# Kernel tuning notes

Hardware: AMD Instinct MI355X
Metric: run time of the kernel (lower is better)

The kernel has to match this reference:

```python
import jax, jax.numpy as jnp
import numpy as np

N = 50000
E = 800000
EMB = 128
HID = 128
HALF = HID // 2

def setup_inputs() -> dict:
    key = jax.random.key(0)
    ks = jax.random.split(key, 16)
    inp = {
        "x": jax.random.normal(ks[0], (N, EMB), dtype=jnp.float32),
        "edge_row": jax.random.randint(ks[1], (E,), 0, N, dtype=jnp.int32),
        "edge_col": jax.random.randint(ks[2], (E,), 0, N, dtype=jnp.int32),
        "edge_vals": jax.random.uniform(ks[3], (E,), dtype=jnp.float32),
        "W_gc0": jax.random.normal(ks[4], (EMB, HID), dtype=jnp.float32) * 0.05,
        "b_gc0": jax.random.normal(ks[5], (HID,), dtype=jnp.float32) * 0.05,
        "W_gc1": jax.random.normal(ks[6], (HID, HID), dtype=jnp.float32) * 0.05,
        "b_gc1": jax.random.normal(ks[7], (HID,), dtype=jnp.float32) * 0.05,
        "Wm1": jax.random.normal(ks[8], (HID, HALF), dtype=jnp.float32) * 0.05,
        "bm1": jax.random.normal(ks[9], (HALF,), dtype=jnp.float32) * 0.05,
        "Wm2": jax.random.normal(ks[10], (HALF, HALF), dtype=jnp.float32) * 0.05,
        "bm2": jax.random.normal(ks[11], (HALF,), dtype=jnp.float32) * 0.05,
        "Wv1": jax.random.normal(ks[12], (HID, HALF), dtype=jnp.float32) * 0.05,
        "bv1": jax.random.normal(ks[13], (HALF,), dtype=jnp.float32) * 0.05,
        "Wv2": jax.random.normal(ks[14], (HALF, HALF), dtype=jnp.float32) * 0.05,
        "bv2": jax.random.normal(ks[15], (HALF,), dtype=jnp.float32) * 0.05,
    }
    return inp

def reference(x, edge_row, edge_col, edge_vals,
              W_gc0, b_gc0, W_gc1, b_gc1,
              Wm1, bm1, Wm2, bm2, Wv1, bv1, Wv2, bv2):
    n = x.shape[0]

    def gcn_layer(h, W, b):
        # support = h @ W  (dense GEMM), then spmm: out[r] += adj[r,c] * support[c]
        support = h @ W                                   # [N, out]
        msgs = edge_vals[:, None] * support[edge_col]      # [E, out]
        agg = jax.ops.segment_sum(msgs, edge_row, num_segments=n)
        return agg + b

    h = jax.nn.relu(gcn_layer(x, W_gc0, b_gc0))
    h = jax.nn.relu(gcn_layer(h, W_gc1, b_gc1))

    mean = jax.nn.relu(h @ Wm1 + bm1) @ Wm2 + bm2
    logvar = jax.nn.relu(h @ Wv1 + bv1) @ Wv2 + bv2
    return mean, logvar
```

## Files before the change

### kernel.cpp

```cpp
#include <hip/hip_runtime.h>
#include <type_traits>


typedef _Float16 half8 __attribute__((ext_vector_type(8)));
typedef float floatx4 __attribute__((ext_vector_type(4)));

#define BCAP 2560
#define CHUNK 2048
#define RB 128

__device__ void gemm_l1(int bid, const float* __restrict__ A,
                        const _Float16* __restrict__ Wswz,
                        _Float16* __restrict__ C0, int n) {
  const int t = threadIdx.x;
  const int lane = t & 63, wave = t >> 6;
  const int quad = lane >> 4, l16 = lane & 15;
  const int r_base = bid * 128 + wave * 32;

  int arow0 = r_base + l16;
  int arow1 = r_base + 16 + l16;
  if (arow0 >= n) arow0 = n - 1;
  if (arow1 >= n) arow1 = n - 1;
  const float* Ap0 = A + (size_t)arow0 * 128 + quad * 8;
  const float* Ap1 = A + (size_t)arow1 * 128 + quad * 8;

  floatx4 acc[2][8] = {};

#pragma unroll
  for (int ks = 0; ks < 4; ++ks) {
    float4 u = *(const float4*)(Ap0 + ks * 32);
    float4 w = *(const float4*)(Ap0 + ks * 32 + 4);
    half8 a0 = half8{(_Float16)u.x, (_Float16)u.y, (_Float16)u.z, (_Float16)u.w,
                     (_Float16)w.x, (_Float16)w.y, (_Float16)w.z, (_Float16)w.w};
    float4 u1 = *(const float4*)(Ap1 + ks * 32);
    float4 w1 = *(const float4*)(Ap1 + ks * 32 + 4);
    half8 a1 = half8{(_Float16)u1.x, (_Float16)u1.y, (_Float16)u1.z, (_Float16)u1.w,
                     (_Float16)w1.x, (_Float16)w1.y, (_Float16)w1.z, (_Float16)w1.w};
#pragma unroll
    for (int nt = 0; nt < 8; ++nt) {
      half8 b = *(const half8*)(Wswz + ((size_t)(ks * 8 + nt) * 64 + lane) * 8);
      acc[0][nt] = __builtin_amdgcn_mfma_f32_16x16x32_f16(a0, b, acc[0][nt], 0, 0, 0);
      acc[1][nt] = __builtin_amdgcn_mfma_f32_16x16x32_f16(a1, b, acc[1][nt], 0, 0, 0);
    }
  }

#pragma unroll
  for (int h = 0; h < 2; ++h) {
#pragma unroll
    for (int nt = 0; nt < 8; ++nt) {
      const int col = nt * 16 + l16;
#pragma unroll
      for (int r = 0; r < 4; ++r) {
        int row = r_base + h * 16 + quad * 4 + r;
        if (row < n) C0[(size_t)row * 128 + col] = (_Float16)acc[h][nt][r];
      }
    }
  }
}

__global__ __launch_bounds__(256)
void buildA_kernel(const int* __restrict__ rows, const int* __restrict__ cols,
                   const float* __restrict__ vals,
                   int* __restrict__ bcur, uint2* __restrict__ bbuf, int e,
                   int binBlocks,
                   const float* __restrict__ w0, const float* __restrict__ w1,
                   const float* __restrict__ wm1, const float* __restrict__ wv1,
                   const float* __restrict__ wm2, const float* __restrict__ wv2,
                   _Float16* __restrict__ d0, _Float16* __restrict__ d1,
                   _Float16* __restrict__ dh1, _Float16* __restrict__ dh2) {
  __shared__ int cnt[392];
  __shared__ int cur[392];
  const int t = threadIdx.x;

  if (blockIdx.x >= binBlocks) {
    int i = (blockIdx.x - binBlocks) * 256 + t;
    if (i >= 65536) return;
    int seg = i >> 14, li = i & 16383;
    int j = li & 7, lane = (li >> 3) & 63, tt = li >> 9;
    int nt = tt & 7, ks = tt >> 3;
    int k = ks * 32 + (lane >> 4) * 8 + j;
    int nn = nt * 16 + (lane & 15);
    float v;
    if (seg == 0)      v = w0[k * 128 + nn];
    else if (seg == 1) v = w1[k * 128 + nn];
    else if (seg == 2) v = (nn < 64) ? wm1[k * 64 + nn] : wv1[k * 64 + (nn - 64)];
    else v = (k < 64 && nn < 64) ? wm2[k * 64 + nn]
           : (k >= 64 && nn >= 64) ? wv2[(k - 64) * 64 + (nn - 64)] : 0.f;
    _Float16* dst = (seg == 0) ? d0 : (seg == 1) ? d1 : (seg == 2) ? dh1 : dh2;
    dst[li] = (_Float16)v;
    return;
  }

  const int lo = blockIdx.x * CHUNK, hi = min(lo + CHUNK, e);
  int myr[8], myc[8];
  float myv[8];
  int nk = 0;
  for (int i = lo + t; i < hi; i += 256, ++nk) {
    myr[nk] = rows[i];
    myc[nk] = cols[i];
    myv[nk] = vals[i];
  }
  for (int j = t; j < 392; j += 256) cnt[j] = 0;
  __syncthreads();
  for (int k = 0; k < nk; ++k)
    atomicAdd(&cnt[myr[k] >> 7], 1);
  __syncthreads();
  for (int j = t; j < 392; j += 256)
    if (cnt[j] > 0) cur[j] = atomicAdd(&bcur[j * 16], cnt[j]);
  __syncthreads();
  for (int k = 0; k < nk; ++k) {
    int r = myr[k];
    int b = r >> 7;
    int p = atomicAdd(&cur[b], 1);
    if (p < BCAP)
      bbuf[(size_t)b * BCAP + p] =
          make_uint2(((unsigned)(r & (RB - 1)) << 16) | (unsigned)myc[k],
                     __float_as_uint(myv[k]));
  }
}

__global__ __launch_bounds__(256)
void buildB_kernel(const uint2* __restrict__ bbuf, const int* __restrict__ bcur,
                   int* __restrict__ row_ptr, int2* __restrict__ s_pack,
                   int nbk, int n, int e_total,
                   const float* __restrict__ x, const _Float16* __restrict__ W0s,
                   _Float16* __restrict__ sup) {
  __shared__ int cnt[RB];
  __shared__ int scn[RB];
  __shared__ int red[256];
  __shared__ int2 stage[BCAP];

  if (blockIdx.x >= nbk) {
    gemm_l1(blockIdx.x - nbk, x, W0s, sup, n);
    return;
  }

  const int b = blockIdx.x, t = threadIdx.x;

  int partial = 0;
  for (int j = t; j < b; j += 256) partial += bcur[j * 16];
  red[t] = partial;
  __syncthreads();
#pragma unroll
  for (int off = 128; off > 0; off >>= 1) {
    if (t < off) red[t] += red[t + off];
    __syncthreads();
  }
  const int base = red[0];

  const int e = min(bcur[b * 16], BCAP);
  const uint2* src = bbuf + (size_t)b * BCAP;

  if (t < RB) cnt[t] = 0;
  __syncthreads();
  for (int i = t; i < e; i += 256)
    atomicAdd(&cnt[(src[i].x >> 16) & (RB - 1)], 1);
  __syncthreads();
  int c = (t < RB) ? cnt[t] : 0;
  if (t < RB) scn[t] = c;
  __syncthreads();
#pragma unroll
  for (int off = 1; off < RB; off <<= 1) {
    int a = (t >= off && t < RB) ? scn[t - off] : 0;
    __syncthreads();
    if (t < RB) scn[t] += a;
    __syncthreads();
  }
  if (t < RB) {
    int excl = scn[t] - c;
    int grow = b * RB + t;
    if (grow < n) row_ptr[grow] = base + excl;
    cnt[t] = excl;
  }
  if (b == 0 && t == 0) row_ptr[n] = e_total;
  __syncthreads();
  for (int i = t; i < e; i += 256) {
    uint2 u = src[i];
    int pos = atomicAdd(&cnt[(u.x >> 16) & (RB - 1)], 1);
    stage[pos] = make_int2((int)(u.x & 0xFFFFu), (int)u.y);
  }
  __syncthreads();
  for (int i = t; i < e; i += 256)
    s_pack[base + i] = stage[i];
}

template<bool HEADS>
__global__ __launch_bounds__(256)
void spmm_fused(const half8* __restrict__ sup, const int* __restrict__ row_ptr,
                const int2* __restrict__ s_pack, const float* __restrict__ gbias,
                const _Float16* __restrict__ W1swz, const _Float16* __restrict__ W2swz,
                const float* __restrict__ hb0, const float* __restrict__ hb1,
                const float* __restrict__ ob0, const float* __restrict__ ob1,
                _Float16* __restrict__ outA, float* __restrict__ outM,
                float* __restrict__ outV, int n) {
  __shared__ _Float16 hs[16][136];
  __shared__ _Float16 ts[HEADS ? 16 : 1][136];
  const int t = threadIdx.x;
  const int g = t >> 4;
  const int l = t & 15;
  int r = blockIdx.x * 16 + g;
  if (r >= n) r = n - 1;
  const int beg = row_ptr[r], end = row_ptr[r + 1];

  float acc[8] = {};
  int i = beg;
  for (; i + 3 < end; i += 4) {
    int2 e0 = s_pack[i], e1 = s_pack[i + 1], e2 = s_pack[i + 2], e3 = s_pack[i + 3];
    half8 g0 = sup[(size_t)e0.x * 16 + l];
    half8 g1 = sup[(size_t)e1.x * 16 + l];
    half8 g2 = sup[(size_t)e2.x * 16 + l];
    half8 g3 = sup[(size_t)e3.x * 16 + l];
    float v0 = __int_as_float(e0.y), v1 = __int_as_float(e1.y);
    float v2 = __int_as_float(e2.y), v3 = __int_as_float(e3.y);
#pragma unroll
    for (int jj = 0; jj < 8; ++jj) acc[jj] = fmaf(v0, (float)g0[jj], acc[jj]);
#pragma unroll
    for (int jj = 0; jj < 8; ++jj) acc[jj] = fmaf(v1, (float)g1[jj], acc[jj]);
#pragma unroll
    for (int jj = 0; jj < 8; ++jj) acc[jj] = fmaf(v2, (float)g2[jj], acc[jj]);
#pragma unroll
    for (int jj = 0; jj < 8; ++jj) acc[jj] = fmaf(v3, (float)g3[jj], acc[jj]);
  }
  for (; i < end; ++i) {
    int2 e0 = s_pack[i];
    float v = __int_as_float(e0.y);
    half8 gg = sup[(size_t)e0.x * 16 + l];
#pragma unroll
    for (int jj = 0; jj < 8; ++jj) acc[jj] = fmaf(v, (float)gg[jj], acc[jj]);
  }

  float4 b0 = *(const float4*)(gbias + 8 * l);
  float4 b1 = *(const float4*)(gbias + 8 * l + 4);
  _Float16* hp = &hs[g][8 * l];
  hp[0] = (_Float16)fmaxf(acc[0] + b0.x, 0.f);
  hp[1] = (_Float16)fmaxf(acc[1] + b0.y, 0.f);
  hp[2] = (_Float16)fmaxf(acc[2] + b0.z, 0.f);
  hp[3] = (_Float16)fmaxf(acc[3] + b0.w, 0.f);
  hp[4] = (_Float16)fmaxf(acc[4] + b1.x, 0.f);
  hp[5] = (_Float16)fmaxf(acc[5] + b1.y, 0.f);
  hp[6] = (_Float16)fmaxf(acc[6] + b1.z, 0.f);
  hp[7] = (_Float16)fmaxf(acc[7] + b1.w, 0.f);
  __syncthreads();

  const int lane = t & 63, wave = t >> 6;
  const int quad = lane >> 4, l16 = lane & 15;
  floatx4 cacc[2] = {{0.f, 0.f, 0.f, 0.f}, {0.f, 0.f, 0.f, 0.f}};
#pragma unroll
  for (int ks = 0; ks < 4; ++ks) {
    half8 a = *(const half8*)&hs[l16][ks * 32 + quad * 8];
#pragma unroll
    for (int nt = 0; nt < 2; ++nt) {
      int ntg = wave * 2 + nt;
      half8 b = *(const half8*)(W1swz + ((size_t)(ks * 8 + ntg) * 64 + lane) * 8);
      cacc[nt] = __builtin_amdgcn_mfma_f32_16x16x32_f16(a, b, cacc[nt], 0, 0, 0);
    }
  }

  if constexpr (!HEADS) {
#pragma unroll
    for (int nt = 0; nt < 2; ++nt) {
      int col = wave * 32 + nt * 16 + l16;
#pragma unroll
      for (int rr = 0; rr < 4; ++rr) {
        int row = blockIdx.x * 16 + quad * 4 + rr;
        if (row < n) outA[(size_t)row * 128 + col] = (_Float16)cacc[nt][rr];
      }
    }
  } else {
#pragma unroll
    for (int nt = 0; nt < 2; ++nt) {
      int col = wave * 32 + nt * 16 + l16;
      float bv = (col < 64) ? hb0[col] : hb1[col - 64];
#pragma unroll
      for (int rr = 0; rr < 4; ++rr)
        ts[quad * 4 + rr][col] = (_Float16)fmaxf(cacc[nt][rr] + bv, 0.f);
    }
    __syncthreads();
    floatx4 oacc[2] = {{0.f, 0.f, 0.f, 0.f}, {0.f, 0.f, 0.f, 0.f}};
#pragma unroll
    for (int ks = 0; ks < 4; ++ks) {
      half8 a = *(const half8*)&ts[l16][ks * 32 + quad * 8];
#pragma unroll
      for (int nt = 0; nt < 2; ++nt) {
        int ntg = wave * 2 + nt;
        half8 b = *(const half8*)(W2swz + ((size_t)(ks * 8 + ntg) * 64 + lane) * 8);
        oacc[nt] = __builtin_amdgcn_mfma_f32_16x16x32_f16(a, b, oacc[nt], 0, 0, 0);
      }
    }
#pragma unroll
    for (int nt = 0; nt < 2; ++nt) {
      int col = wave * 32 + nt * 16 + l16;
      float bv = (col < 64) ? ob0[col] : ob1[col - 64];
#pragma unroll
      for (int rr = 0; rr < 4; ++rr) {
        int row = blockIdx.x * 16 + quad * 4 + rr;
        if (row < n) {
          float v = oacc[nt][rr] + bv;
          if (col < 64) outM[(size_t)row * 64 + col] = v;
          else          outV[(size_t)row * 64 + (col - 64)] = v;
        }
      }
    }
  }
}

extern "C" void kernel_launch(void* const* d_in, const int* in_sizes, int n_in,
                              void* d_out, int out_size, void* d_ws, size_t ws_size,
                              hipStream_t stream) {
  const float* x        = (const float*)d_in[0];
  const int*   edge_row = (const int*)d_in[1];
  const int*   edge_col = (const int*)d_in[2];
  const float* edge_val = (const float*)d_in[3];
  const float* W_gc0 = (const float*)d_in[4];
  const float* b_gc0 = (const float*)d_in[5];
  const float* W_gc1 = (const float*)d_in[6];
  const float* b_gc1 = (const float*)d_in[7];
  const float* Wm1 = (const float*)d_in[8];
  const float* bm1 = (const float*)d_in[9];
  const float* Wm2 = (const float*)d_in[10];
  const float* bm2 = (const float*)d_in[11];
  const float* Wv1 = (const float*)d_in[12];
  const float* bv1 = (const float*)d_in[13];
  const float* Wv2 = (const float*)d_in[14];
  const float* bv2 = (const float*)d_in[15];

  const int N = in_sizes[0] / 128;
  const int E = in_sizes[1];
  const int NBK = (N + RB - 1) / RB;

  char* ws = (char*)d_ws;
  _Float16* bufA16 = (_Float16*)(ws);
  _Float16* bufB16 = (_Float16*)(ws + (size_t)N * 256);
  int2*  s_pack = (int2*)(ws + (size_t)N * 512);
  char*  p = ws + (size_t)N * 512 + (size_t)E * 8;
  int*   row_ptr = (int*)p;           p += 200064;
  int*   bcur    = (int*)p;           p += (size_t)NBK * 64;
  uint2* bbuf    = (uint2*)p;         p += (size_t)NBK * BCAP * 8;
  _Float16* W0s  = (_Float16*)p;      p += 32768;
  _Float16* W1s  = (_Float16*)p;      p += 32768;
  _Float16* Wh1s = (_Float16*)p;      p += 32768;
  _Float16* Wh2s = (_Float16*)p;      p += 32768;

  float* out_mean = (float*)d_out;
  float* out_lvar = out_mean + (size_t)N * 64;

  hipMemsetAsync(bcur, 0, (size_t)NBK * 64, stream);
  const int binBlocks = (E + CHUNK - 1) / CHUNK;
  buildA_kernel<<<binBlocks + 256, 256, 0, stream>>>(
      edge_row, edge_col, edge_val, bcur, bbuf, E, binBlocks,
      W_gc0, W_gc1, Wm1, Wv1, Wm2, Wv2, W0s, W1s, Wh1s, Wh2s);

  const int GB = (N + 127) / 128;
  const int SB = (N + 15) / 16;

  buildB_kernel<<<NBK + GB, 256, 0, stream>>>(bbuf, bcur, row_ptr, s_pack,
                                              NBK, N, E, x, W0s, bufA16);
  spmm_fused<false><<<SB, 256, 0, stream>>>((const half8*)bufA16, row_ptr, s_pack,
                                            b_gc0, W1s, nullptr,
                                            nullptr, nullptr, nullptr, nullptr,
                                            bufB16, nullptr, nullptr, N);
  spmm_fused<true><<<SB, 256, 0, stream>>>((const half8*)bufB16, row_ptr, s_pack,
                                           b_gc1, Wh1s, Wh2s,
                                           bm1, bv1, bm2, bv2,
                                           nullptr, out_mean, out_lvar, N);
}
```

Before: 210.2 us.

## Stage binned edges in LDS with a local counting sort before global scatter

Edge binning now does a block-local counting sort. It runs a shared-memory histogram and a prefix scan, places each edge into an LDS staging buffer ordered by bin, then writes each bin's run to its global slots in contiguous segments. The goal is to replace fully scattered 8-byte global writes with short coalesced runs, and the chunk per block is doubled to make those runs longer. In exchange it re-reads the row indices from global memory, adds a 32 KB LDS stage and several barriers, and launches fewer binning blocks.

Result: slower. 218.1 us (+3.8%).

```diff
diff --git a/kernel.cpp b/kernel.cpp
--- a/kernel.cpp
+++ b/kernel.cpp
@@ -6,8 +6,9 @@
 typedef float floatx4 __attribute__((ext_vector_type(4)));
 
 #define BCAP 2560
-#define CHUNK 2048
+#define CHUNK 4096
 #define RB 128
+#define NBKMAX 392
 
 __device__ void gemm_l1(int bid, const float* __restrict__ A,
                         const _Float16* __restrict__ Wswz,
@@ -68,8 +69,12 @@
                    const float* __restrict__ wm2, const float* __restrict__ wv2,
                    _Float16* __restrict__ d0, _Float16* __restrict__ d1,
                    _Float16* __restrict__ dh1, _Float16* __restrict__ dh2) {
-  __shared__ int cnt[392];
-  __shared__ int cur[392];
+  __shared__ int cnt[NBKMAX];
+  __shared__ int excl[NBKMAX];
+  __shared__ int lcur[NBKMAX];
+  __shared__ int gbase[NBKMAX];
+  __shared__ int sc[512];
+  __shared__ uint2 stage[CHUNK];
   const int t = threadIdx.x;
 
   if (blockIdx.x >= binBlocks) {
@@ -92,30 +97,44 @@
   }
 
   const int lo = blockIdx.x * CHUNK, hi = min(lo + CHUNK, e);
-  int myr[8], myc[8];
-  float myv[8];
-  int nk = 0;
-  for (int i = lo + t; i < hi; i += 256, ++nk) {
-    myr[nk] = rows[i];
-    myc[nk] = cols[i];
-    myv[nk] = vals[i];
-  }
-  for (int j = t; j < 392; j += 256) cnt[j] = 0;
-  __syncthreads();
-  for (int k = 0; k < nk; ++k)
-    atomicAdd(&cnt[myr[k] >> 7], 1);
-  __syncthreads();
-  for (int j = t; j < 392; j += 256)
-    if (cnt[j] > 0) cur[j] = atomicAdd(&bcur[j * 16], cnt[j]);
-  __syncthreads();
-  for (int k = 0; k < nk; ++k) {
-    int r = myr[k];
-    int b = r >> 7;
-    int p = atomicAdd(&cur[b], 1);
-    if (p < BCAP)
-      bbuf[(size_t)b * BCAP + p] =
-          make_uint2(((unsigned)(r & (RB - 1)) << 16) | (unsigned)myc[k],
-                     __float_as_uint(myv[k]));
+  for (int j = t; j < NBKMAX; j += 256) cnt[j] = 0;
+  __syncthreads();
+  for (int i = lo + t; i < hi; i += 256)
+    atomicAdd(&cnt[rows[i] >> 7], 1);
+  __syncthreads();
+  sc[t] = (t < NBKMAX) ? cnt[t] : 0;
+  sc[t + 256] = (t + 256 < NBKMAX) ? cnt[t + 256] : 0;
+  __syncthreads();
+#pragma unroll
+  for (int off = 1; off < 512; off <<= 1) {
+    int a0 = (t >= off) ? sc[t - off] : 0;
+    int a1 = (t + 256 >= off) ? sc[t + 256 - off] : 0;
+    __syncthreads();
+    sc[t] += a0;
+    sc[t + 256] += a1;
+    __syncthreads();
+  }
+  for (int j = t; j < NBKMAX; j += 256) {
+    int ex = sc[j] - cnt[j];
+    excl[j] = ex;
+    lcur[j] = ex;
+    if (cnt[j] > 0) gbase[j] = atomicAdd(&bcur[j * 16], cnt[j]);
+  }
+  __syncthreads();
+  for (int i = lo + t; i < hi; i += 256) {
+    int r = rows[i];
+    int p = atomicAdd(&lcur[r >> 7], 1);
+    stage[p] = make_uint2(((unsigned)r << 16) | (unsigned)cols[i],
+                          __float_as_uint(vals[i]));
+  }
+  __syncthreads();
+  const int tot = hi - lo;
+  for (int i = t; i < tot; i += 256) {
+    uint2 u = stage[i];
+    int b = (int)(u.x >> 16) >> 7;
+    int slot = gbase[b] + (i - excl[b]);
+    if (slot < BCAP)
+      bbuf[(size_t)b * BCAP + slot] = make_uint2(u.x & 0x007FFFFFu, u.y);
   }
 }
 
```
